# Kernel optimization log

Hardware: AMD Instinct MI355X
Metric: run time of the kernel (lower is better)

## Reference

```python
import jax, jax.numpy as jnp
import numpy as np
from jax.scipy.linalg import solve_triangular

EMB = 2048; NKH = 16; NVH = 32; DK = 128; DV = 128
KSZ = 4; EPS = 1e-6; CHUNK = 64
KEY_DIM = NKH * DK; VAL_DIM = NVH * DV
CONV_DIM = 2 * KEY_DIM + VAL_DIM  # q,k (key_dim each) + v (value_dim)
B, S = 1, 4096  # S % CHUNK == 0 -> no padding path


def setup_inputs() -> dict:
    key = jax.random.key(0)
    ks = jax.random.split(key, 7)
    s = 0.02
    return {
        "hidden_states": jax.random.normal(ks[0], (B, S, EMB), jnp.float32),
        "W_qkvz": jax.random.normal(ks[1], (EMB, 2 * KEY_DIM + 2 * VAL_DIM), jnp.float32) * s,
        "W_ba": jax.random.normal(ks[2], (EMB, 2 * NVH), jnp.float32) * s,
        "conv_kernel": jax.random.normal(ks[3], (KSZ, 1, CONV_DIM), jnp.float32) * 0.1,
        "A_log": jnp.log(jax.random.uniform(ks[4], (NVH,), jnp.float32, 1e-9, 16.0)),
        "dt_bias": jnp.ones((NVH,), jnp.float32),
        "norm_weight": jnp.ones((DV,), jnp.float32),
        "W_out": jax.random.normal(ks[5], (VAL_DIM, EMB), jnp.float32) * s,
    }


def _chunk_gated_delta_rule(q, k, v, g, beta):
    """q,k: [B,S,H,DK]; v: [B,S,H,DV]; g,beta: [B,S,H]. Returns [B,S,H,DV]."""
    dt = q.dtype
    prec = jax.lax.Precision.HIGHEST
    q = jnp.transpose(q, (0, 2, 1, 3)).astype(jnp.float32)
    k = jnp.transpose(k, (0, 2, 1, 3)).astype(jnp.float32)
    v = jnp.transpose(v, (0, 2, 1, 3)).astype(jnp.float32)
    beta = jnp.transpose(beta, (0, 2, 1)).astype(jnp.float32)
    g = jnp.transpose(g, (0, 2, 1)).astype(jnp.float32)
    b, h, s, dk = k.shape
    dv = v.shape[-1]
    nc = s // CHUNK
    q = q * jax.lax.rsqrt(jnp.float32(dk))
    v_beta = v * beta[..., None]
    k_beta = k * beta[..., None]
    qc = q.reshape(b, h, nc, CHUNK, dk)
    kc = k.reshape(b, h, nc, CHUNK, dk)
    kbc = k_beta.reshape(b, h, nc, CHUNK, dk)
    vbc = v_beta.reshape(b, h, nc, CHUNK, dv)
    gc = g.reshape(b, h, nc, CHUNK)
    g_cum = jnp.cumsum(gc, axis=-1)                        # [b,h,nc,C]
    g_diff = g_cum[..., :, None] - g_cum[..., None, :]     # [b,h,nc,C,C]
    decay = jnp.exp(jnp.tril(g_diff))
    tri_incl = jnp.triu(jnp.ones((CHUNK, CHUNK), bool), k=0)
    L = -jnp.matmul(kbc, jnp.swapaxes(kc, -1, -2), precision=prec) * decay
    L = jnp.where(tri_incl, 0.0, L)  # strictly lower
    eye = jnp.eye(CHUNK, dtype=jnp.float32)
    # UT transform: original fori_loop forward-substitution == (I - L)^{-1}
    attn = solve_triangular(eye - L, jnp.broadcast_to(eye, L.shape), lower=True)
    v_intra = jnp.matmul(attn, vbc, precision=prec)
    k_cumdecay = jnp.matmul(attn, kbc * jnp.exp(g_cum)[..., None], precision=prec)
    state0 = jnp.zeros((b, h, dk, dv), jnp.float32)
    tri_strict = jnp.triu(jnp.ones((CHUNK, CHUNK), bool), k=1)
    xs = tuple(jnp.moveaxis(t, 2, 0) for t in (qc, kc, v_intra, k_cumdecay, g_cum, decay))

    def scan_body(state, x):
        q_i, k_i, v_i, kcd_i, g_i, dm_i = x
        a_i = jnp.matmul(q_i, jnp.swapaxes(k_i, -1, -2), precision=prec) * dm_i
        a_i = jnp.where(tri_strict, 0.0, a_i)
        v_new = v_i - jnp.matmul(kcd_i, state, precision=prec)
        out_i = jnp.matmul(q_i * jnp.exp(g_i)[..., None], state, precision=prec) \
              + jnp.matmul(a_i, v_new, precision=prec)
        g_last = g_i[..., -1]
        new_state = state * jnp.exp(g_last)[..., None, None] \
            + jnp.matmul(jnp.swapaxes(k_i * jnp.exp(g_last[..., None] - g_i)[..., None], -1, -2),
                         v_new, precision=prec)
        return new_state, out_i

    _, out = jax.lax.scan(scan_body, state0, xs)
    out = jnp.moveaxis(out, 0, 2).reshape(b, h, s, dv)
    return jnp.transpose(out, (0, 2, 1, 3)).astype(dt)


def reference(hidden_states, W_qkvz, W_ba, conv_kernel, A_log, dt_bias, norm_weight, W_out):
    b, s, _ = hidden_states.shape
    vk = NVH // NKH  # v heads per k head
    qkvz = hidden_states @ W_qkvz                          # [b,s,12288]
    ba = hidden_states @ W_ba                              # [b,s,64]
    mixed = qkvz.reshape(b, s, NKH, 2 * DK + 2 * vk * DV)
    q, k, v_raw, z_raw = jnp.split(mixed, [DK, 2 * DK, 2 * DK + vk * DV], axis=3)
    value = v_raw.reshape(b, s, NVH, DV)
    z = z_raw.reshape(b, s, NVH, DV)
    mixed_ba = ba.reshape(b, s, NKH, 2 * vk)
    b_raw, a_raw = jnp.split(mixed_ba, [vk], axis=3)
    b_gate = b_raw.reshape(b, s, NVH)
    a_gate = a_raw.reshape(b, s, NVH)
    # depthwise causal conv over the concatenated q,k,v channels
    qkv = jnp.concatenate([q.reshape(b, s, -1), k.reshape(b, s, -1), value.reshape(b, s, -1)], axis=-1)
    x = jnp.pad(qkv, ((0, 0), (KSZ - 1, 0), (0, 0)))
    conv = jax.lax.conv_general_dilated(x, conv_kernel, (1,), 'VALID',
                                        dimension_numbers=('NWC', 'WIO', 'NWC'),
                                        feature_group_count=CONV_DIM)
    qkv_c = jax.nn.silu(conv.astype(jnp.float32)).astype(hidden_states.dtype)
    q_c, k_c, v_c = jnp.split(qkv_c, [KEY_DIM, 2 * KEY_DIM], axis=-1)
    query = q_c.reshape(b, s, NKH, DK)
    key = k_c.reshape(b, s, NKH, DK)
    value = v_c.reshape(b, s, NVH, DV)
    beta = jax.nn.sigmoid(b_gate)
    g = (-jnp.exp(A_log.astype(jnp.float32))
         * jax.nn.softplus(a_gate.astype(jnp.float32) + dt_bias.astype(jnp.float32))
         ).astype(hidden_states.dtype)
    query = jnp.repeat(query, vk, axis=2)
    key = jnp.repeat(key, vk, axis=2)
    core = _chunk_gated_delta_rule(query, key, value, g, beta)  # [b,s,NVH,DV]
    # gated RMSNorm (Mamba2-style): gate first, then normalize
    xf = core.astype(jnp.float32) * jax.nn.silu(z.astype(jnp.float32))
    var = jnp.mean(xf * xf, axis=-1, keepdims=True)
    xf = xf * jax.lax.rsqrt(var + EPS) * norm_weight
    out = xf.astype(hidden_states.dtype).reshape(b, s, VAL_DIM)
    return out @ W_out
```

## Files before the change

kernel.cpp:

```cpp
#include <hip/hip_runtime.h>


typedef __attribute__((ext_vector_type(8))) __bf16 bf16x8;
typedef __attribute__((ext_vector_type(4))) float f32x4;
typedef __bf16 bf16_t;

#define MFMA_BF16(A, B, C) __builtin_amdgcn_mfma_f32_16x16x32_bf16((A), (B), (C), 0, 0, 0)

__device__ __forceinline__ void async16(const bf16_t* g, bf16_t* l) {
  __builtin_amdgcn_global_load_lds(
      (const __attribute__((address_space(1))) unsigned*)g,
      (__attribute__((address_space(3))) unsigned*)l, 16, 0, 0);
}

__device__ __forceinline__ bf16_t f2bf(float x) {
  unsigned u = __builtin_bit_cast(unsigned, x);
  unsigned r = u + 0x7fffu + ((u >> 16) & 1u);
  unsigned short s = (unsigned short)(r >> 16);
  return __builtin_bit_cast(bf16_t, s);
}
__device__ __forceinline__ float bf2f(bf16_t b) {
  unsigned short s = __builtin_bit_cast(unsigned short, b);
  unsigned u = ((unsigned)s) << 16;
  return __builtin_bit_cast(float, u);
}
__device__ __forceinline__ unsigned packhl(float x) {
  bf16_t h = f2bf(x);
  bf16_t l = f2bf(x - bf2f(h));
  return (((unsigned)__builtin_bit_cast(unsigned short, h)) << 16) |
         (unsigned)__builtin_bit_cast(unsigned short, l);
}
__device__ __forceinline__ float upk(unsigned u) {
  return __builtin_bit_cast(float, u & 0xffff0000u) +
         __builtin_bit_cast(float, u << 16);
}

struct FragPair { bf16x8 hi, lo; };

__device__ __forceinline__ void load8(float v[8], const float* p) {
  float4 a = *(const float4*)p;
  float4 b = *(const float4*)(p + 4);
  v[0] = a.x; v[1] = a.y; v[2] = a.z; v[3] = a.w;
  v[4] = b.x; v[5] = b.y; v[6] = b.z; v[7] = b.w;
}
__device__ __forceinline__ void load8u(unsigned v[8], const unsigned* p) {
  uint4 a = *(const uint4*)p;
  uint4 b = *(const uint4*)(p + 4);
  v[0] = a.x; v[1] = a.y; v[2] = a.z; v[3] = a.w;
  v[4] = b.x; v[5] = b.y; v[6] = b.z; v[7] = b.w;
}
__device__ __forceinline__ FragPair split8(const float v[8]) {
  FragPair f;
#pragma unroll
  for (int j = 0; j < 8; j++) {
    bf16_t h = f2bf(v[j]);
    f.hi[j] = h;
    f.lo[j] = f2bf(v[j] - bf2f(h));
  }
  return f;
}
__device__ __forceinline__ FragPair unpack8(const unsigned v[8]) {
  FragPair f;
#pragma unroll
  for (int j = 0; j < 8; j++) {
    f.hi[j] = __builtin_bit_cast(bf16_t, (unsigned short)(v[j] >> 16));
    f.lo[j] = __builtin_bit_cast(bf16_t, (unsigned short)(v[j] & 0xffffu));
  }
  return f;
}

__global__ void k_cvt(const float* __restrict__ in, bf16_t* __restrict__ out, int n) {
  int i = (blockIdx.x * 256 + threadIdx.x) * 4;
  if (i + 3 < n) {
    float4 v = *(const float4*)(in + i);
    out[i + 0] = f2bf(v.x); out[i + 1] = f2bf(v.y);
    out[i + 2] = f2bf(v.z); out[i + 3] = f2bf(v.w);
  }
}

__global__ void k_transpose_cvt(const float* __restrict__ in, bf16_t* __restrict__ out,
                                int K, int N) {
  __shared__ bf16_t tile[64 * 65];
  int n0 = blockIdx.x * 64, k0 = blockIdx.y * 64;
  int c = threadIdx.x & 63, rg = threadIdx.x >> 6;
#pragma unroll
  for (int rr = 0; rr < 16; rr++) {
    int r = rr * 4 + rg;
    tile[c * 65 + r] = f2bf(in[(size_t)(k0 + r) * N + n0 + c]);
  }
  __syncthreads();
#pragma unroll
  for (int rr = 0; rr < 16; rr++) {
    int r = rr * 4 + rg;
    out[(size_t)(n0 + r) * K + k0 + c] = tile[r * 65 + c];
  }
}

__global__ void k_ktrans(const bf16_t* __restrict__ kb, bf16_t* __restrict__ kbT) {
  __shared__ __align__(16) bf16_t t[128][72];
  int kh = blockIdx.x >> 6, ci = blockIdx.x & 63, s0 = ci * 64;
  int s = threadIdx.x & 63, dg = threadIdx.x >> 6;
  const bf16_t* src = kb + (size_t)(s0 + s) * 2048 + kh * 128 + dg * 32;
#pragma unroll
  for (int j = 0; j < 4; j++) {
    bf16x8 v = *(const bf16x8*)(src + j * 8);
#pragma unroll
    for (int e = 0; e < 8; e++) t[dg * 32 + j * 8 + e][s] = v[e];
  }
  __syncthreads();
  int d = threadIdx.x >> 1, sh = (threadIdx.x & 1) * 32;
  bf16_t* dst = kbT + ((size_t)blockIdx.x * 128 + d) * 64 + sh;
#pragma unroll
  for (int j = 0; j < 4; j++)
    *(bf16x8*)(dst + j * 8) = *(const bf16x8*)(&t[d][sh + j * 8]);
}

__global__ __launch_bounds__(256) void k_gemm(const bf16_t* __restrict__ A,
                                              const bf16_t* __restrict__ BT,
                                              float* __restrict__ C, int M, int N, int K) {
  __shared__ __align__(16) bf16_t sA[128 * 32];
  __shared__ __align__(16) bf16_t sB[128 * 32];
  const int tid = threadIdx.x;
  const int lane = tid & 63, w = tid >> 6;
  const int quad = lane >> 4, l15 = lane & 15;
  const int m0 = blockIdx.y * 128, n0 = blockIdx.x * 128;
  const int wm = (w >> 1) * 64, wn = (w & 1) * 64;
  f32x4 acc[4][4];
#pragma unroll
  for (int a = 0; a < 4; a++)
#pragma unroll
    for (int b = 0; b < 4; b++) { f32x4 z = {0.f, 0.f, 0.f, 0.f}; acc[a][b] = z; }
  const int sb = (lane & 7) ^ ((lane >> 3) & 7);
  const int srow = ((tid >> 3) << 1) + (sb >> 2);
  const int scol = (sb & 3) * 8;
  const bf16_t* gA = A + (size_t)(m0 + srow) * K + scol;
  const bf16_t* gB = BT + (size_t)(n0 + srow) * K + scol;
  bf16_t* lA = sA + w * 512;
  bf16_t* lB = sB + w * 512;
  const int rh = l15 >> 1;
  const int bs = (((l15 & 1) << 2) + quad) ^ rh;
  const int foff = rh * 64 + bs * 8;
  for (int kt = 0; kt < K; kt += 32) {
    async16(gA + kt, lA);
    async16(gA + (size_t)64 * K + kt, lA + 2048);
    async16(gB + kt, lB);
    async16(gB + (size_t)64 * K + kt, lB + 2048);
    __syncthreads();
    bf16x8 af[4], bfv[4];
#pragma unroll
    for (int t = 0; t < 4; t++) {
      af[t]  = *(const bf16x8*)(sA + ((wm >> 1) + t * 8) * 64 + foff);
      bfv[t] = *(const bf16x8*)(sB + ((wn >> 1) + t * 8) * 64 + foff);
    }
#pragma unroll
    for (int mt = 0; mt < 4; mt++)
#pragma unroll
      for (int nt = 0; nt < 4; nt++)
        acc[mt][nt] = MFMA_BF16(af[mt], bfv[nt], acc[mt][nt]);
    __syncthreads();
  }
#pragma unroll
  for (int mt = 0; mt < 4; mt++)
#pragma unroll
    for (int nt = 0; nt < 4; nt++) {
      int row0 = m0 + wm + mt * 16 + quad * 4;
      int col = n0 + wn + nt * 16 + l15;
#pragma unroll
      for (int r = 0; r < 4; r++)
        C[(size_t)(row0 + r) * N + col] = acc[mt][nt][r];
    }
}

__global__ __launch_bounds__(512, 2) void k_gemm_qkvz(const bf16_t* __restrict__ A,
                                                      const bf16_t* __restrict__ BT,
                                                      bf16_t* __restrict__ qkvb,
                                                      bf16_t* __restrict__ zb,
                                                      int M, int N, int K) {
  __shared__ __align__(16) bf16_t sL[2 * 4 * 8192];
  const int tid = threadIdx.x;
  const int lane = tid & 63, w = tid >> 6;
  const int quad = lane >> 4, l15 = lane & 15;

  int id = blockIdx.y * gridDim.x + blockIdx.x;
  const int xcd = id & 7, jj = id >> 3;
  const int bx = xcd * 6 + (jj % 6), by = jj / 6;
  const int m0 = by * 256, n0 = bx * 256;
  const int wm = (w >> 2) * 128, wn = (w & 3) * 64;
  const int hA = (w >> 2);
  const int hB = 2 + ((w & 3) >> 1);
  const int brow0 = wn & 64;

  f32x4 acc[8][4];
#pragma unroll
  for (int m = 0; m < 8; m++)
#pragma unroll
    for (int n = 0; n < 4; n++) { f32x4 z = {0.f, 0.f, 0.f, 0.f}; acc[m][n] = z; }

  const int rbase = w * 8 + (lane >> 3);
  const int sq = (lane & 7) ^ ((lane >> 3) & 7);
  const bf16_t* gb[4];
  gb[0] = A + (size_t)(m0 + rbase) * K + sq * 8;
  gb[1] = A + (size_t)(m0 + 128 + rbase) * K + sq * 8;
  gb[2] = BT + (size_t)(n0 + rbase) * K + sq * 8;
  gb[3] = BT + (size_t)(n0 + 128 + rbase) * K + sq * 8;
  const size_t j64 = (size_t)64 * K;

  bf16x8 afr[4][2], bf01[2][2], bf23[2][2];
  const int NI = K >> 7;

  auto stg = [&](int cb, int h, int kt) {
    const bf16_t* s = gb[h] + (size_t)kt * 64;
    bf16_t* d = sL + (cb * 4 + h) * 8192 + w * 512;
    async16(s, d);
    async16(s + j64, d + 4096);
  };
  auto ldA = [&](int cb, int mg) {
    const bf16_t* base = sL + (cb * 4 + hA) * 8192;
#pragma unroll
    for (int m = 0; m < 4; m++)
#pragma unroll
      for (int ks = 0; ks < 2; ks++)
        afr[m][ks] = *(const bf16x8*)(base + (mg * 64 + m * 16 + l15) * 64 +
                                      (((ks * 4 + quad) ^ (l15 & 7)) * 8));
  };
  auto ldB = [&](int cb, int ng, bf16x8 (&bf)[2][2]) {
    const bf16_t* base = sL + (cb * 4 + hB) * 8192;
#pragma unroll
    for (int n = 0; n < 2; n++)
#pragma unroll
      for (int ks = 0; ks < 2; ks++)
        bf[n][ks] = *(const bf16x8*)(base + (brow0 + ng * 32 + n * 16 + l15) * 64 +
                                     (((ks * 4 + quad) ^ (l15 & 7)) * 8));
  };
  auto mm = [&](int mg, int ng, bf16x8 (&bf)[2][2]) {
    __builtin_amdgcn_s_setprio(1);
#pragma unroll
    for (int m = 0; m < 4; m++)
#pragma unroll
      for (int n = 0; n < 2; n++)
#pragma unroll
        for (int ks = 0; ks < 2; ks++)
          acc[mg * 4 + m][ng * 2 + n] =
              MFMA_BF16(afr[m][ks], bf[n][ks], acc[mg * 4 + m][ng * 2 + n]);
    __builtin_amdgcn_s_setprio(0);
  };

#define PH_OPEN()                                           \
  do {                                                      \
    __builtin_amdgcn_sched_barrier(0);                      \
    __builtin_amdgcn_s_barrier();                           \
    asm volatile("s_waitcnt lgkmcnt(0)" ::: "memory");      \
    __builtin_amdgcn_sched_barrier(0);                      \
  } while (0)
#define PH_CLOSE()                                          \
  do {                                                      \
    __builtin_amdgcn_sched_barrier(0);                      \
    __builtin_amdgcn_s_barrier();                           \
  } while (0)

#pragma unroll
  for (int h = 0; h < 4; h++) stg(0, h, 0);
  stg(1, 2, 1);
  stg(1, 3, 1);
  asm volatile("s_waitcnt vmcnt(4)" ::: "memory");
  __builtin_amdgcn_s_barrier();

  for (int i = 0; i < NI; ++i) {
    const int k2 = 2 * i;
    const bool more = (i + 1 < NI);
    ldA(0, 0); ldB(0, 0, bf01);
    stg(1, 0, k2 + 1);
    asm volatile("s_waitcnt lgkmcnt(8)" ::: "memory");
    PH_OPEN(); mm(0, 0, bf01); PH_CLOSE();
    ldB(0, 1, bf23);
    stg(1, 1, k2 + 1);
    PH_OPEN(); mm(0, 1, bf23); PH_CLOSE();
    ldA(0, 1);
    if (more) stg(0, 2, k2 + 2);
    PH_OPEN(); mm(1, 0, bf01); PH_CLOSE();
    if (more) {
      stg(0, 3, k2 + 2);
      asm volatile("s_waitcnt vmcnt(4)" ::: "memory");
    } else {
      asm volatile("s_waitcnt vmcnt(0)" ::: "memory");
    }
    PH_OPEN(); mm(1, 1, bf23); PH_CLOSE();
    ldA(1, 0); ldB(1, 0, bf01);
    if (more) stg(0, 0, k2 + 2);
    asm volatile("s_waitcnt lgkmcnt(8)" ::: "memory");
    PH_OPEN(); mm(0, 0, bf01); PH_CLOSE();
    ldB(1, 1, bf23);
    if (more) stg(0, 1, k2 + 2);
    PH_OPEN(); mm(0, 1, bf23); PH_CLOSE();
    ldA(1, 1);
    if (more) stg(1, 2, k2 + 3);
    PH_OPEN(); mm(1, 0, bf01); PH_CLOSE();
    if (more) {
      stg(1, 3, k2 + 3);
      asm volatile("s_waitcnt vmcnt(4)" ::: "memory");
    } else {
      asm volatile("s_waitcnt vmcnt(0)" ::: "memory");
    }
    PH_OPEN(); mm(1, 1, bf23); PH_CLOSE();
  }
#undef PH_OPEN
#undef PH_CLOSE

#pragma unroll
  for (int n = 0; n < 4; n++) {
    int c = n0 + wn + n * 16 + l15;
    int kh = c / 768;
    int rr = c - kh * 768;
    bool isz = (rr >= 512);
    bf16_t* dst = isz ? zb : qkvb;
    size_t stride = isz ? 4096 : 8192;
    size_t coff = isz ? (size_t)(kh * 256 + (rr - 512)) : (size_t)(kh * 512 + rr);
#pragma unroll
    for (int m = 0; m < 8; m++) {
      int row0 = m0 + wm + m * 16 + quad * 4;
#pragma unroll
      for (int r = 0; r < 4; r++)
        dst[(size_t)(row0 + r) * stride + coff] = f2bf(acc[m][n][r]);
    }
  }
}

__global__ __launch_bounds__(256) void k_ba(const float* __restrict__ hs,
                                            const float* __restrict__ Wba,
                                            const float* __restrict__ A_log,
                                            const float* __restrict__ dtb,
                                            float* __restrict__ g, float* __restrict__ beta) {
  __shared__ float sH[4][2048];
  int s0 = blockIdx.x * 32;
  int c = threadIdx.x & 63, sg = threadIdx.x >> 6;
  for (int rg = 0; rg < 8; rg++) {
    __syncthreads();
    for (int i = threadIdx.x; i < 2048; i += 256) {
      int r = i >> 9, kk = (i & 511) * 4;
      *(float4*)(&sH[r][kk]) = *(const float4*)(hs + (size_t)(s0 + rg * 4 + r) * 2048 + kk);
    }
    __syncthreads();
    float dot = 0.f;
    for (int kk = 0; kk < 2048; kk += 4) {
      float4 hv = *(const float4*)(&sH[sg][kk]);
      dot += hv.x * Wba[(kk + 0) * 64 + c] + hv.y * Wba[(kk + 1) * 64 + c] +
             hv.z * Wba[(kk + 2) * 64 + c] + hv.w * Wba[(kk + 3) * 64 + c];
    }
    int s = s0 + rg * 4 + sg;
    int hh = c >> 2, j = c & 3;
    if (j < 2) {
      int vh = hh * 2 + j;
      beta[s * 32 + vh] = 1.f / (1.f + __expf(-dot));
    } else {
      int vh = hh * 2 + (j - 2);
      float x = dot + dtb[vh];
      float sp = (x > 20.f) ? x : log1pf(__expf(x));
      g[s * 32 + vh] = -__expf(A_log[vh]) * sp;
    }
  }
}

__global__ void k_conv(const bf16_t* __restrict__ qkvb, const float* __restrict__ ck,
                       bf16_t* __restrict__ qb, bf16_t* __restrict__ kb,
                       bf16_t* __restrict__ vb) {
  int c = blockIdx.x * 256 + threadIdx.x;
  int s0 = blockIdx.y * 128;
  int col, dstc, dstride;
  bf16_t* dst;
  float scale = 1.0f;
  if (c < 2048) {
    int hh = c >> 7, d = c & 127;
    col = hh * 512 + d; dst = qb; dstc = c; dstride = 2048;
    scale = 0.08838834764831845f;
  } else if (c < 4096) {
    int cc = c - 2048, hh = cc >> 7, d = cc & 127;
    col = hh * 512 + 128 + d; dst = kb; dstc = cc; dstride = 2048;
  } else {
    int cc = c - 4096, vh = cc >> 7, d = cc & 127;
    col = (vh >> 1) * 512 + 256 + (vh & 1) * 128 + d; dst = vb; dstc = cc; dstride = 4096;
  }
  float w0 = ck[c], w1 = ck[8192 + c], w2 = ck[2 * 8192 + c], w3 = ck[3 * 8192 + c];
  float x0 = 0.f, x1 = 0.f, x2 = 0.f;
  if (s0 >= 3) {
    x0 = bf2f(qkvb[(size_t)(s0 - 3) * 8192 + col]);
    x1 = bf2f(qkvb[(size_t)(s0 - 2) * 8192 + col]);
    x2 = bf2f(qkvb[(size_t)(s0 - 1) * 8192 + col]);
  }
  for (int s = s0; s < s0 + 128; s++) {
    float x3 = bf2f(qkvb[(size_t)s * 8192 + col]);
    float y = w0 * x0 + w1 * x1 + w2 * x2 + w3 * x3;
    y = y / (1.f + __expf(-y));
    dst[(size_t)s * dstride + dstc] = f2bf(y * scale);
    x0 = x1; x1 = x2; x2 = x3;
  }
}

__global__ __launch_bounds__(256) void k_phaseA(const bf16_t* __restrict__ kb,
                                                const bf16_t* __restrict__ vb,
                                                const float* __restrict__ g,
                                                const float* __restrict__ beta,
                                                float* __restrict__ vi,
                                                bf16_t* __restrict__ kcdn) {
  __shared__ __align__(16) char smem[36608];
  float* sGc = (float*)smem;
  float* sBt = (float*)(smem + 256);
  float* sBE = (float*)(smem + 512);
  float* sP  = (float*)(smem + 768);
  bf16_t* sQ  = (bf16_t*)(smem + 18176);
  bf16_t* sQT = (bf16_t*)(smem + 27392);
  bf16_t* sVT = (bf16_t*)(smem + 18176);
  bf16_t* sKT = (bf16_t*)(smem + 27392);

  const int tid = threadIdx.x, lane = tid & 63, w = tid >> 6;
  const int quad = lane >> 4, l15 = lane & 15;
  const int h = blockIdx.x >> 6, ci = blockIdx.x & 63;
  const int kh = h >> 1, s0 = ci * 64;
  const int m = w * 16 + l15;

  if (tid < 64) {
    float gv = g[(size_t)(s0 + tid) * 32 + h];
    float bv = beta[(size_t)(s0 + tid) * 32 + h];
#pragma unroll
    for (int off = 1; off < 64; off <<= 1) {
      float t = __shfl_up(gv, off, 64);
      if (tid >= off) gv += t;
    }
    sGc[tid] = gv; sBt[tid] = bv; sBE[tid] = bv * __expf(gv);
  }
  __syncthreads();

  const bf16_t* krow = kb + (size_t)s0 * 2048 + kh * 128;
  bf16x8 ak[4];
#pragma unroll
  for (int ks = 0; ks < 4; ks++)
    ak[ks] = *(const bf16x8*)(krow + (size_t)m * 2048 + ks * 32 + quad * 8);
  f32x4 accL[4];
#pragma unroll
  for (int nt = 0; nt < 4; nt++) { f32x4 z = {0.f, 0.f, 0.f, 0.f}; accL[nt] = z; }
#pragma unroll
  for (int nt = 0; nt < 4; nt++)
#pragma unroll
    for (int ks = 0; ks < 4; ks++) {
      bf16x8 bk = *(const bf16x8*)(krow + (size_t)(nt * 16 + l15) * 2048 + ks * 32 + quad * 8);
      accL[nt] = MFMA_BF16(ak[ks], bk, accL[nt]);
    }
#pragma unroll
  for (int nt = 0; nt < 4; nt++) {
    int j = nt * 16 + l15;
#pragma unroll
    for (int r = 0; r < 4; r++) {
      int i = w * 16 + quad * 4 + r;
      float Lij = (i > j) ? (-accL[nt][r] * sBt[i] * __expf(sGc[i] - sGc[j])) : 0.f;
      sP[i * 68 + j] = ((i == j) ? 1.f : 0.f) + Lij;
      bf16_t q16 = f2bf(Lij);
      sQ[i * 72 + j] = q16;
      sQT[j * 72 + i] = q16;
    }
  }
  __syncthreads();

  for (int it = 0; it < 5; it++) {
    f32x4 accQ[4];
#pragma unroll
    for (int nt = 0; nt < 4; nt++) { f32x4 z = {0.f, 0.f, 0.f, 0.f}; accQ[nt] = z; }
    bf16x8 qa[2];
#pragma unroll
    for (int ks = 0; ks < 2; ks++)
      qa[ks] = *(const bf16x8*)(sQ + m * 72 + ks * 32 + quad * 8);
#pragma unroll
    for (int nt = 0; nt < 4; nt++)
#pragma unroll
      for (int ks = 0; ks < 2; ks++) {
        bf16x8 qv = *(const bf16x8*)(sQT + (nt * 16 + l15) * 72 + ks * 32 + quad * 8);
        accQ[nt] = MFMA_BF16(qa[ks], qv, accQ[nt]);
      }
    __syncthreads();
#pragma unroll
    for (int nt = 0; nt < 4; nt++) {
      int j = nt * 16 + l15;
#pragma unroll
      for (int r = 0; r < 4; r++) {
        int i = w * 16 + quad * 4 + r;
        bf16_t q16 = f2bf(accQ[nt][r]);
        sQ[i * 72 + j] = q16;
        sQT[j * 72 + i] = q16;
      }
    }
    __syncthreads();
    f32x4 accP[4];
#pragma unroll
    for (int nt = 0; nt < 4; nt++) { f32x4 z = {0.f, 0.f, 0.f, 0.f}; accP[nt] = z; }
    FragPair pa[2];
#pragma unroll
    for (int ks = 0; ks < 2; ks++) {
      float v[8];
      load8(v, sP + m * 68 + ks * 32 + quad * 8);
      pa[ks] = split8(v);
    }
#pragma unroll
    for (int nt = 0; nt < 4; nt++)
#pragma unroll
      for (int ks = 0; ks < 2; ks++) {
        bf16x8 qv = *(const bf16x8*)(sQT + (nt * 16 + l15) * 72 + ks * 32 + quad * 8);
        accP[nt] = MFMA_BF16(pa[ks].hi, qv, accP[nt]);
        accP[nt] = MFMA_BF16(pa[ks].lo, qv, accP[nt]);
      }
#pragma unroll
    for (int nt = 0; nt < 4; nt++) {
      int j = nt * 16 + l15;
#pragma unroll
      for (int r = 0; r < 4; r++) {
        int i = w * 16 + quad * 4 + r;
        sP[i * 68 + j] += accP[nt][r];
      }
    }
  }

  FragPair paV[2], paK[2];
#pragma unroll
  for (int ks = 0; ks < 2; ks++) {
    float v[8];
    load8(v, sP + m * 68 + ks * 32 + quad * 8);
    float vv[8], vk[8];
#pragma unroll
    for (int jj = 0; jj < 8; jj++) {
      int i = ks * 32 + quad * 8 + jj;
      vv[jj] = v[jj] * sBt[i];
      vk[jj] = v[jj] * sBE[i];
    }
    paV[ks] = split8(vv);
    paK[ks] = split8(vk);
  }

  for (int hf = 0; hf < 2; hf++) {
    __syncthreads();
    {
      int sidx = tid & 63, dg = tid >> 6;
      const bf16_t* vsrc = vb + (size_t)(s0 + sidx) * 4096 + h * 128 + hf * 64 + dg * 16;
      const bf16_t* ksrc = kb + (size_t)(s0 + sidx) * 2048 + kh * 128 + hf * 64 + dg * 16;
      bf16x8 v0 = *(const bf16x8*)vsrc;
      bf16x8 v1 = *(const bf16x8*)(vsrc + 8);
      bf16x8 k0 = *(const bf16x8*)ksrc;
      bf16x8 k1 = *(const bf16x8*)(ksrc + 8);
#pragma unroll
      for (int e = 0; e < 8; e++) {
        sVT[(dg * 16 + e) * 72 + sidx] = v0[e];
        sVT[(dg * 16 + 8 + e) * 72 + sidx] = v1[e];
        sKT[(dg * 16 + e) * 72 + sidx] = k0[e];
        sKT[(dg * 16 + 8 + e) * 72 + sidx] = k1[e];
      }
    }
    __syncthreads();
    f32x4 accV[4], accK[4];
#pragma unroll
    for (int nt = 0; nt < 4; nt++) {
      f32x4 z = {0.f, 0.f, 0.f, 0.f};
      accV[nt] = z; accK[nt] = z;
    }
#pragma unroll
    for (int nt = 0; nt < 4; nt++)
#pragma unroll
      for (int ks = 0; ks < 2; ks++) {
        bf16x8 bv = *(const bf16x8*)(sVT + (nt * 16 + l15) * 72 + ks * 32 + quad * 8);
        accV[nt] = MFMA_BF16(paV[ks].hi, bv, accV[nt]);
        accV[nt] = MFMA_BF16(paV[ks].lo, bv, accV[nt]);
        bf16x8 bk = *(const bf16x8*)(sKT + (nt * 16 + l15) * 72 + ks * 32 + quad * 8);
        accK[nt] = MFMA_BF16(paK[ks].hi, bk, accK[nt]);
        accK[nt] = MFMA_BF16(paK[ks].lo, bk, accK[nt]);
      }
#pragma unroll
    for (int nt = 0; nt < 4; nt++) {
      int col = hf * 64 + nt * 16 + l15;
#pragma unroll
      for (int r = 0; r < 4; r++) {
        int row = w * 16 + quad * 4 + r;
        size_t o = ((size_t)h * 4096 + s0 + row) * 128 + col;
        vi[o] = accV[nt][r];
        kcdn[o] = f2bf(-accK[nt][r]);
      }
    }
  }
}

__global__ __launch_bounds__(256) void k_phaseB(const bf16_t* __restrict__ qb,
                                                const bf16_t* __restrict__ kbT,
                                                const float* __restrict__ g,
                                                const float* __restrict__ vi,
                                                const bf16_t* __restrict__ kcdn,
                                                bf16_t* __restrict__ vnT,
                                                bf16_t* __restrict__ outp) {
  __shared__ __align__(16) char smem[13312];
  float* sGc2 = (float*)smem;
  unsigned* sSTp = (unsigned*)(smem + 512);
  unsigned* sVTp = (unsigned*)(smem + 8960);
  const int tid = threadIdx.x, lane = tid & 63, w = tid >> 6;
  const int quad = lane >> 4, l15 = lane & 15;
  const int h = blockIdx.x >> 3, cg = blockIdx.x & 7;
  const int kh = h >> 1, col0 = cg * 16;
  const int m = w * 16 + l15;

  for (int i = tid; i < 16 * 132; i += 256) sSTp[i] = 0u;
  if (tid < 64) {
    float gv = g[(size_t)tid * 32 + h];
#pragma unroll
    for (int off = 1; off < 64; off <<= 1) {
      float t = __shfl_up(gv, off, 64);
      if (tid >= off) gv += t;
    }
    sGc2[tid] = gv;
  }
  __syncthreads();

  for (int ci = 0; ci < 64; ci++) {
    const int s0 = ci * 64;
    const float* sGc = sGc2 + (ci & 1) * 64;

    const bf16_t* kcrow = kcdn + ((size_t)h * 4096 + s0 + m) * 128;
    const bf16_t* qrow = qb + (size_t)(s0 + m) * 2048 + kh * 128;
    bf16x8 a1[4], a2[4], kT[2][2];
#pragma unroll
    for (int d = 0; d < 4; d++) {
      a1[d] = *(const bf16x8*)(kcrow + d * 32 + quad * 8);
      a2[d] = *(const bf16x8*)(qrow + d * 32 + quad * 8);
    }
#pragma unroll
    for (int mi = 0; mi < 2; mi++)
#pragma unroll
      for (int ks = 0; ks < 2; ks++)
        kT[mi][ks] = *(const bf16x8*)(kbT + ((size_t)(kh * 64 + ci) * 128 +
                                             w * 32 + mi * 16 + l15) * 64 + ks * 32 + quad * 8);
    const int colg = col0 + l15;
    size_t vbase = ((size_t)h * 4096 + s0 + w * 16 + quad * 4) * 128 + colg;
    f32x4 accV = {vi[vbase], vi[vbase + 128], vi[vbase + 256], vi[vbase + 384]};
    f32x4 accO = {0.f, 0.f, 0.f, 0.f};
#pragma unroll
    for (int d = 0; d < 4; d++) {
      unsigned u[8];
      load8u(u, sSTp + l15 * 132 + d * 32 + quad * 8);
      FragPair B = unpack8(u);
      accV = MFMA_BF16(a1[d], B.hi, accV);
      accV = MFMA_BF16(a1[d], B.lo, accV);
      accO = MFMA_BF16(a2[d], B.hi, accO);
      accO = MFMA_BF16(a2[d], B.lo, accO);
    }
    const float gl = sGc[63];
    {
      bf16_t* vout = vnT + ((size_t)(h * 64 + ci) * 128 + colg) * 64 + w * 16 + quad * 4;
      bf16_t* oout = outp + vbase;
      ushort4 vv;
      unsigned pk[4];
      unsigned short vb_[4];
#pragma unroll
      for (int r = 0; r < 4; r++) {
        float gr = sGc[w * 16 + quad * 4 + r];
        oout[(size_t)r * 128] = f2bf(accO[r] * __expf(gr));
        vb_[r] = __builtin_bit_cast(unsigned short, f2bf(accV[r]));
        pk[r] = packhl(accV[r] * __expf(gl - gr));
      }
      vv.x = vb_[0]; vv.y = vb_[1]; vv.z = vb_[2]; vv.w = vb_[3];
      *(ushort4*)vout = vv;
      uint4 pv; pv.x = pk[0]; pv.y = pk[1]; pv.z = pk[2]; pv.w = pk[3];
      *(uint4*)(sVTp + l15 * 68 + w * 16 + quad * 4) = pv;
    }
    __syncthreads();

    f32x4 accD[2];
#pragma unroll
    for (int mi = 0; mi < 2; mi++) { f32x4 z = {0.f, 0.f, 0.f, 0.f}; accD[mi] = z; }
#pragma unroll
    for (int ks = 0; ks < 2; ks++) {
      unsigned u[8];
      load8u(u, sVTp + l15 * 68 + ks * 32 + quad * 8);
      FragPair Bv = unpack8(u);
#pragma unroll
      for (int mi = 0; mi < 2; mi++) {
        accD[mi] = MFMA_BF16(kT[mi][ks], Bv.hi, accD[mi]);
        accD[mi] = MFMA_BF16(kT[mi][ks], Bv.lo, accD[mi]);
      }
    }
    float egl = __expf(gl);
#pragma unroll
    for (int mi = 0; mi < 2; mi++) {
      int row0 = w * 32 + mi * 16 + quad * 4;
      unsigned* ps = sSTp + l15 * 132 + row0;
      uint4 old4 = *(uint4*)ps;
      uint4 nu;
      nu.x = packhl(upk(old4.x) * egl + accD[mi][0]);
      nu.y = packhl(upk(old4.y) * egl + accD[mi][1]);
      nu.z = packhl(upk(old4.z) * egl + accD[mi][2]);
      nu.w = packhl(upk(old4.w) * egl + accD[mi][3]);
      *(uint4*)ps = nu;
    }
    if (ci + 1 < 64 && tid < 64) {
      float gv = g[(size_t)((ci + 1) * 64 + tid) * 32 + h];
#pragma unroll
      for (int off = 1; off < 64; off <<= 1) {
        float t = __shfl_up(gv, off, 64);
        if (tid >= off) gv += t;
      }
      sGc2[((ci + 1) & 1) * 64 + tid] = gv;
    }
    __syncthreads();
  }
}

__global__ __launch_bounds__(256) void k_phaseC(const bf16_t* __restrict__ qb,
                                                const bf16_t* __restrict__ kb,
                                                const float* __restrict__ g,
                                                const bf16_t* __restrict__ vnT,
                                                const bf16_t* __restrict__ outp,
                                                const bf16_t* __restrict__ zb,
                                                const float* __restrict__ nw,
                                                bf16_t* __restrict__ xf) {
  __shared__ __align__(16) char smem[17664];
  float* sGc = (float*)smem;
  unsigned* sAp = (unsigned*)(smem + 256);
  const int tid = threadIdx.x, lane = tid & 63, w = tid >> 6;
  const int quad = lane >> 4, l15 = lane & 15;
  const int h = blockIdx.x >> 6, ci = blockIdx.x & 63;
  const int kh = h >> 1, s0 = ci * 64;
  const int m = w * 16 + l15;

  if (tid < 64) {
    float gv = g[(size_t)(s0 + tid) * 32 + h];
#pragma unroll
    for (int off = 1; off < 64; off <<= 1) {
      float t = __shfl_up(gv, off, 64);
      if (tid >= off) gv += t;
    }
    sGc[tid] = gv;
  }
  __syncthreads();

  const bf16_t* qrow = qb + (size_t)s0 * 2048 + kh * 128;
  const bf16_t* krow = kb + (size_t)s0 * 2048 + kh * 128;
  bf16x8 aq[4];
#pragma unroll
  for (int ks = 0; ks < 4; ks++)
    aq[ks] = *(const bf16x8*)(qrow + (size_t)m * 2048 + ks * 32 + quad * 8);
  f32x4 accA[4];
#pragma unroll
  for (int nt = 0; nt < 4; nt++) { f32x4 z = {0.f, 0.f, 0.f, 0.f}; accA[nt] = z; }
#pragma unroll
  for (int nt = 0; nt < 4; nt++)
#pragma unroll
    for (int ks = 0; ks < 4; ks++) {
      bf16x8 bk = *(const bf16x8*)(krow + (size_t)(nt * 16 + l15) * 2048 + ks * 32 + quad * 8);
      accA[nt] = MFMA_BF16(aq[ks], bk, accA[nt]);
    }
#pragma unroll
  for (int nt = 0; nt < 4; nt++) {
    int j = nt * 16 + l15;
#pragma unroll
    for (int r = 0; r < 4; r++) {
      int i = w * 16 + quad * 4 + r;
      float a = (i >= j) ? accA[nt][r] * __expf(sGc[i] - sGc[j]) : 0.f;
      sAp[i * 68 + j] = packhl(a);
    }
  }
  __syncthreads();

  FragPair Aa[2];
#pragma unroll
  for (int ks = 0; ks < 2; ks++) {
    unsigned u[8];
    load8u(u, sAp + m * 68 + ks * 32 + quad * 8);
    Aa[ks] = unpack8(u);
  }
  f32x4 accO[8];
#pragma unroll
  for (int nt = 0; nt < 8; nt++) {
    size_t base = ((size_t)h * 4096 + s0 + w * 16 + quad * 4) * 128 + nt * 16 + l15;
    f32x4 z;
    z[0] = bf2f(outp[base]); z[1] = bf2f(outp[base + 128]);
    z[2] = bf2f(outp[base + 256]); z[3] = bf2f(outp[base + 384]);
    accO[nt] = z;
  }
#pragma unroll
  for (int nt = 0; nt < 8; nt++)
#pragma unroll
    for (int ks = 0; ks < 2; ks++) {
      bf16x8 bv = *(const bf16x8*)(vnT + ((size_t)(h * 64 + ci) * 128 + nt * 16 + l15) * 64 +
                                   ks * 32 + quad * 8);
      accO[nt] = MFMA_BF16(Aa[ks].hi, bv, accO[nt]);
      accO[nt] = MFMA_BF16(Aa[ks].lo, bv, accO[nt]);
    }

  float xv[8][4];
  float ss[4] = {0.f, 0.f, 0.f, 0.f};
#pragma unroll
  for (int nt = 0; nt < 8; nt++) {
    int dv = nt * 16 + l15;
#pragma unroll
    for (int r = 0; r < 4; r++) {
      int s = s0 + w * 16 + quad * 4 + r;
      float z = bf2f(zb[(size_t)s * 4096 + h * 128 + dv]);
      float gate = z / (1.f + __expf(-z));
      float val = accO[nt][r] * gate;
      xv[nt][r] = val;
      ss[r] += val * val;
    }
  }
#pragma unroll
  for (int off = 1; off < 16; off <<= 1) {
#pragma unroll
    for (int r = 0; r < 4; r++) ss[r] += __shfl_xor(ss[r], off, 64);
  }
  float rs[4];
#pragma unroll
  for (int r = 0; r < 4; r++) rs[r] = rsqrtf(ss[r] * (1.f / 128.f) + 1e-6f);
#pragma unroll
  for (int nt = 0; nt < 8; nt++) {
    int dv = nt * 16 + l15;
    float nwv = nw[dv];
#pragma unroll
    for (int r = 0; r < 4; r++) {
      int s = s0 + w * 16 + quad * 4 + r;
      xf[(size_t)s * 4096 + h * 128 + dv] = f2bf(xv[nt][r] * rs[r] * nwv);
    }
  }
}

extern "C" void kernel_launch(void* const* d_in, const int* in_sizes, int n_in,
                              void* d_out, int out_size, void* d_ws, size_t ws_size,
                              hipStream_t stream) {
  const float* hs = (const float*)d_in[0];
  const float* Wqkvz = (const float*)d_in[1];
  const float* Wba = (const float*)d_in[2];
  const float* convk = (const float*)d_in[3];
  const float* A_log = (const float*)d_in[4];
  const float* dtb = (const float*)d_in[5];
  const float* nw = (const float*)d_in[6];
  const float* Wout = (const float*)d_in[7];
  float* out = (float*)d_out;
  char* ws = (char*)d_ws;

  const size_t NEED = 252706816u;
  if (ws_size < NEED) return;

  bf16_t* hsbf = (bf16_t*)(ws + 0);
  bf16_t* wqkT = (bf16_t*)(ws + 16777216);
  bf16_t* qb   = (bf16_t*)(ws + 0);
  bf16_t* kb   = (bf16_t*)(ws + 16777216);
  bf16_t* vb   = (bf16_t*)(ws + 33554432);
  bf16_t* vnT  = (bf16_t*)(ws + 33554432);
  bf16_t* qkvb = (bf16_t*)(ws + 67108864);
  float*  vi   = (float*)(ws + 67108864);
  bf16_t* xf   = (bf16_t*)(ws + 67108864);
  bf16_t* zb   = (bf16_t*)(ws + 134217728);
  float*  gbuf = (float*)(ws + 167772160);
  float*  bbuf = (float*)(ws + 168296448);
  bf16_t* kcdn = (bf16_t*)(ws + 168820736);
  bf16_t* woutT= (bf16_t*)(ws + 168820736);
  bf16_t* outp = (bf16_t*)(ws + 202375168);
  bf16_t* kbT  = (bf16_t*)(ws + 235929600);

  k_cvt<<<8192, 256, 0, stream>>>(hs, hsbf, 4096 * 2048);
  k_transpose_cvt<<<dim3(192, 32), 256, 0, stream>>>(Wqkvz, wqkT, 2048, 12288);
  k_gemm_qkvz<<<dim3(48, 16), 512, 0, stream>>>(hsbf, wqkT, qkvb, zb,
                                                4096, 12288, 2048);
  k_ba<<<128, 256, 0, stream>>>(hs, Wba, A_log, dtb, gbuf, bbuf);
  k_conv<<<dim3(32, 32), 256, 0, stream>>>(qkvb, convk, qb, kb, vb);
  k_ktrans<<<1024, 256, 0, stream>>>(kb, kbT);
  k_phaseA<<<2048, 256, 0, stream>>>(kb, vb, gbuf, bbuf, vi, kcdn);
  k_phaseB<<<256, 256, 0, stream>>>(qb, kbT, gbuf, vi, kcdn, vnT, outp);
  k_phaseC<<<2048, 256, 0, stream>>>(qb, kb, gbuf, vnT, outp, zb, nw, xf);
  k_transpose_cvt<<<dim3(32, 64), 256, 0, stream>>>(Wout, woutT, 4096, 2048);
  k_gemm<<<dim3(16, 32), 256, 0, stream>>>(xf, woutT, out, 4096, 2048, 4096);
}
```

Before: 1.022 ms.

## Double-buffer MFMA register fragments and halve barriers in the QKVZ GEMM loop

The QKVZ projection GEMM main loop now keeps two register sets for the A and B fragments. The LDS reads for the next phase are issued before the current phase's MFMAs, so shared-memory latency overlaps with matrix math. Each phase now uses one barrier instead of an open/close pair, and the explicit lgkmcnt waits are dropped in favour of compiler-inserted waits. The async-copy staging order and the vmcnt thresholds are adjusted to fit. This uses more VGPRs and makes the LDS buffer-reuse hazards more delicate to get right.

New measurement: 1.265 ms. +23.7%, slower.

```diff
diff --git a/kernel.cpp b/kernel.cpp
--- a/kernel.cpp
+++ b/kernel.cpp
@@ -205,7 +205,7 @@
   gb[3] = BT + (size_t)(n0 + 128 + rbase) * K + sq * 8;
   const size_t j64 = (size_t)64 * K;
 
-  bf16x8 afr[4][2], bf01[2][2], bf23[2][2];
+  bf16x8 afA[4][2], afB[4][2], bfA[2][2], bfB[2][2];
   const int NI = K >> 7;
 
   auto stg = [&](int cb, int h, int kt) {
@@ -214,25 +214,26 @@
     async16(s, d);
     async16(s + j64, d + 4096);
   };
-  auto ldA = [&](int cb, int mg) {
+  auto ldA = [&](int cb, int mg, bf16x8 (&dst)[4][2]) {
     const bf16_t* base = sL + (cb * 4 + hA) * 8192;
 #pragma unroll
     for (int m = 0; m < 4; m++)
 #pragma unroll
       for (int ks = 0; ks < 2; ks++)
-        afr[m][ks] = *(const bf16x8*)(base + (mg * 64 + m * 16 + l15) * 64 +
+        dst[m][ks] = *(const bf16x8*)(base + (mg * 64 + m * 16 + l15) * 64 +
                                       (((ks * 4 + quad) ^ (l15 & 7)) * 8));
   };
-  auto ldB = [&](int cb, int ng, bf16x8 (&bf)[2][2]) {
+  auto ldB = [&](int cb, int ng, bf16x8 (&dst)[2][2]) {
     const bf16_t* base = sL + (cb * 4 + hB) * 8192;
 #pragma unroll
     for (int n = 0; n < 2; n++)
 #pragma unroll
       for (int ks = 0; ks < 2; ks++)
-        bf[n][ks] = *(const bf16x8*)(base + (brow0 + ng * 32 + n * 16 + l15) * 64 +
-                                     (((ks * 4 + quad) ^ (l15 & 7)) * 8));
+        dst[n][ks] = *(const bf16x8*)(base + (brow0 + ng * 32 + n * 16 + l15) * 64 +
+                                      (((ks * 4 + quad) ^ (l15 & 7)) * 8));
   };
-  auto mm = [&](int mg, int ng, bf16x8 (&bf)[2][2]) {
+  auto mm = [&](int mg, int ng, bf16x8 (&A4)[4][2], bf16x8 (&B2)[2][2]) {
+    __builtin_amdgcn_sched_barrier(0);
     __builtin_amdgcn_s_setprio(1);
 #pragma unroll
     for (int m = 0; m < 4; m++)
@@ -241,70 +242,70 @@
 #pragma unroll
         for (int ks = 0; ks < 2; ks++)
           acc[mg * 4 + m][ng * 2 + n] =
-              MFMA_BF16(afr[m][ks], bf[n][ks], acc[mg * 4 + m][ng * 2 + n]);
+              MFMA_BF16(A4[m][ks], B2[n][ks], acc[mg * 4 + m][ng * 2 + n]);
     __builtin_amdgcn_s_setprio(0);
+    __builtin_amdgcn_sched_barrier(0);
   };
 
-#define PH_OPEN()                                           \
-  do {                                                      \
-    __builtin_amdgcn_sched_barrier(0);                      \
-    __builtin_amdgcn_s_barrier();                           \
-    asm volatile("s_waitcnt lgkmcnt(0)" ::: "memory");      \
-    __builtin_amdgcn_sched_barrier(0);                      \
+#define BARSB()                       \
+  do {                                \
+    __builtin_amdgcn_s_barrier();     \
+    __builtin_amdgcn_sched_barrier(0);\
   } while (0)
-#define PH_CLOSE()                                          \
-  do {                                                      \
-    __builtin_amdgcn_sched_barrier(0);                      \
-    __builtin_amdgcn_s_barrier();                           \
-  } while (0)
-
-#pragma unroll
-  for (int h = 0; h < 4; h++) stg(0, h, 0);
-  stg(1, 2, 1);
-  stg(1, 3, 1);
+
+  stg(0, 0, 0); stg(0, 1, 0); stg(0, 2, 0); stg(0, 3, 0);
+  stg(1, 2, 1); stg(1, 3, 1);
   asm volatile("s_waitcnt vmcnt(4)" ::: "memory");
   __builtin_amdgcn_s_barrier();
+  ldA(0, 0, afA); ldB(0, 0, bfA);
 
   for (int i = 0; i < NI; ++i) {
     const int k2 = 2 * i;
     const bool more = (i + 1 < NI);
-    ldA(0, 0); ldB(0, 0, bf01);
+    BARSB();
+    ldB(0, 1, bfB);
     stg(1, 0, k2 + 1);
-    asm volatile("s_waitcnt lgkmcnt(8)" ::: "memory");
-    PH_OPEN(); mm(0, 0, bf01); PH_CLOSE();
-    ldB(0, 1, bf23);
+    mm(0, 0, afA, bfA);
+    BARSB();
+    ldA(0, 1, afB);
     stg(1, 1, k2 + 1);
-    PH_OPEN(); mm(0, 1, bf23); PH_CLOSE();
-    ldA(0, 1);
-    if (more) stg(0, 2, k2 + 2);
-    PH_OPEN(); mm(1, 0, bf01); PH_CLOSE();
+    mm(0, 1, afA, bfB);
+    BARSB();
     if (more) {
-      stg(0, 3, k2 + 2);
-      asm volatile("s_waitcnt vmcnt(4)" ::: "memory");
+      stg(0, 2, k2 + 2);
+      asm volatile("s_waitcnt vmcnt(2)" ::: "memory");
     } else {
       asm volatile("s_waitcnt vmcnt(0)" ::: "memory");
     }
-    PH_OPEN(); mm(1, 1, bf23); PH_CLOSE();
-    ldA(1, 0); ldB(1, 0, bf01);
+    mm(1, 0, afB, bfA);
+    BARSB();
+    ldA(1, 0, afA); ldB(1, 0, bfA);
+    if (more) stg(0, 3, k2 + 2);
+    mm(1, 1, afB, bfB);
+    BARSB();
+    ldB(1, 1, bfB);
     if (more) stg(0, 0, k2 + 2);
-    asm volatile("s_waitcnt lgkmcnt(8)" ::: "memory");
-    PH_OPEN(); mm(0, 0, bf01); PH_CLOSE();
-    ldB(1, 1, bf23);
+    mm(0, 0, afA, bfA);
+    BARSB();
+    ldA(1, 1, afB);
     if (more) stg(0, 1, k2 + 2);
-    PH_OPEN(); mm(0, 1, bf23); PH_CLOSE();
-    ldA(1, 1);
-    if (more) stg(1, 2, k2 + 3);
-    PH_OPEN(); mm(1, 0, bf01); PH_CLOSE();
+    mm(0, 1, afA, bfB);
+    BARSB();
     if (more) {
-      stg(1, 3, k2 + 3);
-      asm volatile("s_waitcnt vmcnt(4)" ::: "memory");
+      stg(1, 2, k2 + 3);
+      asm volatile("s_waitcnt vmcnt(2)" ::: "memory");
     } else {
       asm volatile("s_waitcnt vmcnt(0)" ::: "memory");
     }
-    PH_OPEN(); mm(1, 1, bf23); PH_CLOSE();
-  }
-#undef PH_OPEN
-#undef PH_CLOSE
+    mm(1, 0, afB, bfA);
+    BARSB();
+    if (more) {
+      ldA(0, 0, afA); ldB(0, 0, bfA);
+      stg(1, 3, k2 + 3);
+    }
+    mm(1, 1, afB, bfB);
+  }
+#undef BARSB
 
 #pragma unroll
   for (int n = 0; n < 4; n++) {
```
